# Performance work log

Hardware: AMD Instinct MI355X
Metric: run time of the kernel (lower is better)

## Reference

```python
import jax, jax.numpy as jnp
import numpy as np


def avg_pool_2x2(x):
    # x: [B, H, W, C] -> [B, H//2, W//2, C], non-overlapping 2x2 mean (Keras AveragePooling2D default)
    B, H, W, C = x.shape
    return x.reshape(B, H // 2, 2, W // 2, 2, C).mean(axis=(2, 4))


def setup_inputs() -> dict:
    key = jax.random.key(0)
    k1, k2, k3, k4, k5 = jax.random.split(key, 5)
    B, H, W, C = 16, 64, 64, 512
    x = jax.random.normal(k1, (B, H, W, C), dtype=jnp.float32)
    Wf = jax.random.normal(k2, (C, C // 8), dtype=jnp.float32) * 0.02
    Wg = jax.random.normal(k3, (C, C // 8), dtype=jnp.float32) * 0.02
    Wh = jax.random.normal(k4, (C, C // 2), dtype=jnp.float32) * 0.02
    Wo = jax.random.normal(k5, (C // 2, C), dtype=jnp.float32) * 0.02
    return {"x": x, "Wf": Wf, "Wg": Wg, "Wh": Wh, "Wo": Wo}


def reference(x, Wf, Wg, Wh, Wo):
    B, H, W, C = x.shape
    # 1x1 convs are per-pixel matmuls over channels
    f = jnp.einsum('bhwc,cd->bhwd', x, Wf).reshape(B, H * W, C // 8)          # queries
    xp = avg_pool_2x2(x)                                                      # [B,H/2,W/2,C]
    g = jnp.einsum('bhwc,cd->bhwd', xp, Wg).reshape(B, H * W // 4, C // 8)    # keys
    h = jnp.einsum('bhwc,cd->bhwd', xp, Wh).reshape(B, H * W // 4, C // 2)    # values
    attn = jax.nn.softmax(jnp.einsum('bqd,bkd->bqk', f, g), axis=-1)          # [B, HW, HW/4]
    y = jnp.einsum('bqk,bkd->bqd', attn, h).reshape(B, H, W, C // 2)
    out = jnp.einsum('bhwd,dc->bhwc', y, Wo) + x                              # residual
    return out
```

## Files before the change

kernel.cpp:

```cpp
#include <hip/hip_runtime.h>


#define DEVI static __device__ __forceinline__

typedef float f32x4  __attribute__((ext_vector_type(4)));
typedef float f32x16 __attribute__((ext_vector_type(16)));
typedef short bf16x8 __attribute__((ext_vector_type(8)));

DEVI short f2bf(float f) {
  union { float f; unsigned u; } v; v.f = f;
  unsigned r = v.u + 0x7FFFu + ((v.u >> 16) & 1u);
  return (short)(r >> 16);
}
DEVI float b2f(short s) {
  union { unsigned u; float f; } v; v.u = ((unsigned)(unsigned short)s) << 16; return v.f;
}
DEVI unsigned cvtpk(float lo, float hi) {
  unsigned r;
  asm("v_cvt_pk_bf16_f32 %0, %1, %2" : "=v"(r) : "v"(lo), "v"(hi));
  return r;
}
DEVI f32x4 mfma16(bf16x8 a, bf16x8 b, f32x4 c) {
  return __builtin_amdgcn_mfma_f32_16x16x32_bf16(a, b, c, 0, 0, 0);
}
DEVI f32x16 mfma32(bf16x8 a, bf16x8 b, f32x16 c) {
  return __builtin_amdgcn_mfma_f32_32x32x16_bf16(a, b, c, 0, 0, 0);
}
DEVI void gload16(const short* gsrc, short* lds) {
  __builtin_amdgcn_global_load_lds(
      (const __attribute__((address_space(1))) void*)gsrc,
      (__attribute__((address_space(3))) void*)lds, 16, 0, 0);
}

__global__ __launch_bounds__(256) void prep_weights(
    const float* __restrict__ Wf, const float* __restrict__ Wg,
    const float* __restrict__ Wh, const float* __restrict__ Wo,
    short* __restrict__ WfT, short* __restrict__ WgT,
    short* __restrict__ WhT, short* __restrict__ WoT) {
  int i = blockIdx.x * 256 + threadIdx.x;
  const float* src; short* dst; int K, N, e;
  if (i < 32768)       { src = Wf; dst = WfT; K = 512; N = 64;  e = i; }
  else if (i < 65536)  { src = Wg; dst = WgT; K = 512; N = 64;  e = i - 32768; }
  else if (i < 196608) { src = Wh; dst = WhT; K = 512; N = 256; e = i - 65536; }
  else                 { src = Wo; dst = WoT; K = 256; N = 512; e = i - 196608; }
  int n = e / K, k = e - n * K;
  dst[e] = f2bf(src[(long)k * N + n]);
}

template<bool SRC_F32>
DEVI void stage64(short* lds, const void* gsrc, int rows, int stride, int tid) {
  const int chunks = rows * 8;
  for (int c = tid; c < chunks; c += 256) {
    int row = c >> 3, slot = c & 7;
    int dstb = row*128 + ((slot ^ (row & 7)) << 4);
    if (SRC_F32) {
      const float* s = (const float*)gsrc + (long)row*stride + slot*8;
      float4 u0 = *(const float4*)s;
      float4 u1 = *(const float4*)(s + 4);
      union { unsigned u[4]; bf16x8 v; } pk;
      pk.u[0] = cvtpk(u0.x, u0.y); pk.u[1] = cvtpk(u0.z, u0.w);
      pk.u[2] = cvtpk(u1.x, u1.y); pk.u[3] = cvtpk(u1.z, u1.w);
      *(bf16x8*)((char*)lds + dstb) = pk.v;
    } else {
      *(bf16x8*)((char*)lds + dstb) =
          *(const bf16x8*)((const short*)gsrc + (long)row*stride + slot*8);
    }
  }
}

template<bool A_F32, bool POOL>
__global__ __launch_bounds__(256) void gemm_k512(const void* __restrict__ A,
    const short* __restrict__ BT, short* __restrict__ C, int Nfull,
    short* __restrict__ xp) {
  __shared__ short As[128*64];
  __shared__ short Bs[64*64];
  const int m0 = blockIdx.x * 128;
  const int n0 = blockIdx.y * 64;
  const int tid = threadIdx.x, w = tid >> 6, lane = tid & 63;
  const int l15 = lane & 15, lhi = lane >> 4;
  const int wr = w >> 1, wc = w & 1;
  f32x4 acc[4][2] = {};
  for (int kt = 0; kt < 8; ++kt) {
    const int k0 = kt * 64;
    if constexpr (A_F32)
      stage64<true >(As, (const float*)A + (long)m0*512 + k0, 128, 512, tid);
    else
      stage64<false>(As, (const short*)A + (long)m0*512 + k0, 128, 512, tid);
    stage64<false>(Bs, BT + (long)n0*512 + k0, 64, 512, tid);
    __syncthreads();
    if constexpr (POOL) {
      const long pr0 = (long)(m0 >> 12)*1024 + ((m0 & 4095) >> 7)*32;
      int wp = tid >> 3, cs = tid & 7;
      const char* Ab = (const char*)As;
      bf16x8 v00 = *(const bf16x8*)(Ab + (2*wp  )*128 + ((cs ^ ((2*wp  )&7))<<4));
      bf16x8 v01 = *(const bf16x8*)(Ab + (2*wp+1)*128 + ((cs ^ ((2*wp+1)&7))<<4));
      bf16x8 v10 = *(const bf16x8*)(Ab + (64+2*wp)*128 + ((cs ^ ((2*wp  )&7))<<4));
      bf16x8 v11 = *(const bf16x8*)(Ab + (65+2*wp)*128 + ((cs ^ ((2*wp+1)&7))<<4));
      float s[8];
      #pragma unroll
      for (int j = 0; j < 8; ++j)
        s[j] = 0.25f*(b2f(v00[j])+b2f(v01[j])+b2f(v10[j])+b2f(v11[j]));
      union { unsigned u[4]; bf16x8 v; } pk;
      pk.u[0] = cvtpk(s[0], s[1]); pk.u[1] = cvtpk(s[2], s[3]);
      pk.u[2] = cvtpk(s[4], s[5]); pk.u[3] = cvtpk(s[6], s[7]);
      *(bf16x8*)(xp + (pr0 + wp)*512 + k0 + cs*8) = pk.v;
    }
    bf16x8 af[4][2], bfr[2][2];
    #pragma unroll
    for (int mi = 0; mi < 4; ++mi)
      #pragma unroll
      for (int ks = 0; ks < 2; ++ks) {
        int m = wr*64 + mi*16 + l15;
        int slot = lhi + ks*4;
        af[mi][ks] = *(const bf16x8*)((const char*)As + m*128 + ((slot ^ (m & 7)) << 4));
      }
    #pragma unroll
    for (int ni = 0; ni < 2; ++ni)
      #pragma unroll
      for (int ks = 0; ks < 2; ++ks) {
        int n = wc*32 + ni*16 + l15;
        int slot = lhi + ks*4;
        bfr[ni][ks] = *(const bf16x8*)((const char*)Bs + n*128 + ((slot ^ (n & 7)) << 4));
      }
    #pragma unroll
    for (int ks = 0; ks < 2; ++ks)
      #pragma unroll
      for (int mi = 0; mi < 4; ++mi)
        #pragma unroll
        for (int ni = 0; ni < 2; ++ni)
          acc[mi][ni] = mfma16(af[mi][ks], bfr[ni][ks], acc[mi][ni]);
    __syncthreads();
  }
  #pragma unroll
  for (int mi = 0; mi < 4; ++mi)
    #pragma unroll
    for (int ni = 0; ni < 2; ++ni)
      #pragma unroll
      for (int r = 0; r < 4; ++r) {
        long row = m0 + wr*64 + mi*16 + lhi*4 + r;
        int col = n0 + wc*32 + ni*16 + l15;
        C[row * (long)Nfull + col] = f2bf(acc[mi][ni][r]);
      }
}

__global__ __launch_bounds__(256) void transpose_h(const short* __restrict__ h,
                                                   short* __restrict__ hT) {
  __shared__ short t[64][72];
  const int k0 = blockIdx.x * 64, n0 = blockIdx.y * 64, b = blockIdx.z;
  const int tid = threadIdx.x;
  {
    int row = tid >> 2, cch = (tid & 3) * 16;
    const short* src = h + ((long)b*1024 + k0 + row) * 256 + n0 + cch;
    *(bf16x8*)&t[row][cch]     = *(const bf16x8*)src;
    *(bf16x8*)&t[row][cch + 8] = *(const bf16x8*)(src + 8);
  }
  __syncthreads();
  {
    int n = tid >> 2, kch = (tid & 3) * 16;
    bf16x8 lo, hi;
    #pragma unroll
    for (int j = 0; j < 8; ++j) { lo[j] = t[kch + j][n]; hi[j] = t[kch + 8 + j][n]; }
    short* dst = hT + ((long)b*256 + n0 + n) * 1024 + k0 + kch;
    *(bf16x8*)dst       = lo;
    *(bf16x8*)(dst + 8) = hi;
  }
}

__global__ __launch_bounds__(256, 2) void attn_kernel(const short* __restrict__ f,
    const short* __restrict__ g, const short* __restrict__ hT,
    const short* __restrict__ WoT, const float* __restrict__ x,
    float* __restrict__ out) {
  extern __shared__ __align__(16) char smem[];
  const int b = blockIdx.y, q0 = blockIdx.x * 128;
  const int tid = threadIdx.x, w = tid >> 6, lane = tid & 63;
  const int l31 = lane & 31, hi = lane >> 5;

  bf16x8 fq[4];
  {
    const short* frow = f + ((long)b*4096 + q0 + w*32 + l31) * 64;
    #pragma unroll
    for (int ks = 0; ks < 4; ++ks) fq[ks] = *(const bf16x8*)(frow + ks*16 + hi*8);
  }

  f32x16 acc2[8] = {};
  float rsq = 0.f;

  auto stage = [&](int buf, int kt) {
    const int k0 = kt * 64;
    short* gbuf = (short*)(smem + buf*8192);
    short* hbuf = (short*)(smem + 16384 + buf*32768);
    #pragma unroll
    for (int it = 0; it < 2; ++it) {
      int c = it*256 + w*64 + lane;
      int row = c >> 3, gslot = (c & 7) ^ (row & 7);
      gload16(g + ((long)b*1024 + k0 + row)*64 + gslot*8, gbuf + (it*256 + w*64)*8);
    }
    #pragma unroll
    for (int it = 0; it < 8; ++it) {
      int c = it*256 + w*64 + lane;
      int row = c >> 3, gslot = (c & 7) ^ (row & 7);
      gload16(hT + ((long)b*256 + row)*1024 + k0 + gslot*8, hbuf + (it*256 + w*64)*8);
    }
  };

  stage(0, 0);
  int cur = 0;
  for (int kt = 0; kt < 16; ++kt) {
    if (kt < 15) {
      stage(cur ^ 1, kt + 1);
      asm volatile("s_waitcnt vmcnt(10)" ::: "memory");
    } else {
      asm volatile("s_waitcnt vmcnt(0)" ::: "memory");
    }
    __builtin_amdgcn_s_barrier();
    const char* gcur = (const char*)(smem + cur*8192);
    const char* hcur = (const char*)(smem + 16384 + cur*32768);
    bf16x8 pa[4];
    #pragma unroll
    for (int kc2 = 0; kc2 < 2; ++kc2) {
      f32x16 s2 = {};
      #pragma unroll
      for (int ks = 0; ks < 4; ++ks) {
        int key = kc2*32 + l31;
        bf16x8 gb = *(const bf16x8*)(gcur + key*128 + (((ks*2 + hi) ^ (l31 & 7)) << 4));
        s2 = mfma32(gb, fq[ks], s2);
      }
      #pragma unroll
      for (int fh = 0; fh < 2; ++fh) {
        const int G = fh*8;
        float e0 = __expf(s2[G+0]), e1 = __expf(s2[G+1]);
        float e2 = __expf(s2[G+2]), e3 = __expf(s2[G+3]);
        float e4 = __expf(s2[G+4]), e5 = __expf(s2[G+5]);
        float e6 = __expf(s2[G+6]), e7 = __expf(s2[G+7]);
        rsq += ((e0 + e1) + (e2 + e3)) + ((e4 + e5) + (e6 + e7));
        unsigned a0 = cvtpk(e0, e1), a1 = cvtpk(e2, e3);
        unsigned b0 = cvtpk(e4, e5), b1 = cvtpk(e6, e7);
        asm volatile("v_permlane32_swap_b32 %0, %1" : "+v"(b0), "+v"(a0));
        asm volatile("v_permlane32_swap_b32 %0, %1" : "+v"(b1), "+v"(a1));
        union { unsigned u[4]; bf16x8 v; } pk;
        pk.u[0] = a0; pk.u[1] = a1; pk.u[2] = b0; pk.u[3] = b1;
        pa[kc2*2 + fh] = pk.v;
      }
    }
    __builtin_amdgcn_s_setprio(1);
    #pragma unroll
    for (int ks = 0; ks < 4; ++ks) {
      #pragma unroll
      for (int nc2 = 0; nc2 < 8; ++nc2) {
        int n = nc2*32 + l31;
        bf16x8 hb = *(const bf16x8*)(hcur + n*128 + (((ks*2 + hi) ^ (l31 & 7)) << 4));
        acc2[nc2] = mfma32(hb, pa[ks], acc2[nc2]);
      }
    }
    __builtin_amdgcn_s_setprio(0);
    __builtin_amdgcn_s_barrier();
    cur ^= 1;
  }
  rsq += __shfl_xor(rsq, 32);
  float ri = 1.f / rsq;
  bf16x8 yB[16];
  #pragma unroll
  for (int nc2 = 0; nc2 < 8; ++nc2) {
    #pragma unroll
    for (int fh = 0; fh < 2; ++fh) {
      const int G = fh*8;
      unsigned a0 = cvtpk(acc2[nc2][G+0]*ri, acc2[nc2][G+1]*ri);
      unsigned a1 = cvtpk(acc2[nc2][G+2]*ri, acc2[nc2][G+3]*ri);
      unsigned b0 = cvtpk(acc2[nc2][G+4]*ri, acc2[nc2][G+5]*ri);
      unsigned b1 = cvtpk(acc2[nc2][G+6]*ri, acc2[nc2][G+7]*ri);
      asm volatile("v_permlane32_swap_b32 %0, %1" : "+v"(b0), "+v"(a0));
      asm volatile("v_permlane32_swap_b32 %0, %1" : "+v"(b1), "+v"(a1));
      union { unsigned u[4]; bf16x8 v; } pk;
      pk.u[0] = a0; pk.u[1] = a1; pk.u[2] = b0; pk.u[3] = b1;
      yB[nc2*2 + fh] = pk.v;
    }
  }
  const long qrow = (long)b*4096 + q0 + w*32 + l31;
  const float* xrow = x + qrow*512;
  float* orow = out + qrow*512;
  for (int cc2 = 0; cc2 < 16; ++cc2) {
    f32x16 ao0 = {}, ao1 = {};
    #pragma unroll
    for (int ns2 = 0; ns2 < 8; ++ns2) {
      bf16x8 wo0 = *(const bf16x8*)(WoT + (cc2*32 + l31)*256 + (2*ns2  )*16 + hi*8);
      bf16x8 wo1 = *(const bf16x8*)(WoT + (cc2*32 + l31)*256 + (2*ns2+1)*16 + hi*8);
      ao0 = mfma32(wo0, yB[2*ns2  ], ao0);
      ao1 = mfma32(wo1, yB[2*ns2+1], ao1);
    }
    #pragma unroll
    for (int g2 = 0; g2 < 4; ++g2) {
      int c = cc2*32 + g2*8 + hi*4;
      float4 xv = *(const float4*)(xrow + c);
      float4 ov;
      ov.x = ao0[g2*4+0] + ao1[g2*4+0] + xv.x;
      ov.y = ao0[g2*4+1] + ao1[g2*4+1] + xv.y;
      ov.z = ao0[g2*4+2] + ao1[g2*4+2] + xv.z;
      ov.w = ao0[g2*4+3] + ao1[g2*4+3] + xv.w;
      *(float4*)(orow + c) = ov;
    }
  }
}

extern "C" void kernel_launch(void* const* d_in, const int* in_sizes, int n_in,
                              void* d_out, int out_size, void* d_ws, size_t ws_size,
                              hipStream_t stream) {
  const float* x  = (const float*)d_in[0];
  const float* Wf = (const float*)d_in[1];
  const float* Wg = (const float*)d_in[2];
  const float* Wh = (const float*)d_in[3];
  const float* Wo = (const float*)d_in[4];
  float* out = (float*)d_out;

  short* xp  = (short*)d_ws;
  short* fb  = xp  + (long)16*1024*512;
  short* gb  = fb  + (long)65536*64;
  short* hb  = gb  + (long)16384*64;
  short* hTb = hb  + (long)16384*256;
  short* WfT = hTb + (long)16*256*1024;
  short* WgT = WfT + 64*512;
  short* WhT = WgT + 64*512;
  short* WoT = WhT + 256*512;

  hipFuncSetAttribute((const void*)attn_kernel,
                      hipFuncAttributeMaxDynamicSharedMemorySize, 81920);

  prep_weights<<<1536, 256, 0, stream>>>(Wf, Wg, Wh, Wo, WfT, WgT, WhT, WoT);
  gemm_k512<true , true ><<<dim3(512, 1), 256, 0, stream>>>((const void*)x,  WfT, fb, 64,  xp);
  gemm_k512<false, false><<<dim3(128, 1), 256, 0, stream>>>((const void*)xp, WgT, gb, 64,  nullptr);
  gemm_k512<false, false><<<dim3(128, 4), 256, 0, stream>>>((const void*)xp, WhT, hb, 256, nullptr);
  transpose_h <<<dim3(16, 4, 16), 256, 0, stream>>>(hb, hTb);
  attn_kernel <<<dim3(32, 16), 256, 81920, stream>>>(fb, gb, hTb, WoT, x, out);
}
```

Measured before the change: 203.2 us.

## Split output projection into separate GEMM kernel and fold log2e into queries

The Wo projection and residual add move out of the attention kernel into a new gemm_out kernel. The attention kernel now writes the normalized y as bf16 to a workspace buffer, and gemm_out stages y tiles in LDS, preloads Wo fragments and prefetches the x residual. The query projection output is also scaled by log2(e), so the softmax can use exp2f instead of __expf. This is meant to shorten the attention kernel's tail and improve overlap in the projection, at the cost of an extra y round trip through memory and one more kernel launch.

New measurement: 258.4 us. 1.27x slower.

```diff
diff --git a/kernel.cpp b/kernel.cpp
--- a/kernel.cpp
+++ b/kernel.cpp
@@ -71,7 +71,7 @@
 template<bool A_F32, bool POOL>
 __global__ __launch_bounds__(256) void gemm_k512(const void* __restrict__ A,
     const short* __restrict__ BT, short* __restrict__ C, int Nfull,
-    short* __restrict__ xp) {
+    short* __restrict__ xp, float cscale) {
   __shared__ short As[128*64];
   __shared__ short Bs[64*64];
   const int m0 = blockIdx.x * 128;
@@ -139,7 +139,7 @@
       for (int r = 0; r < 4; ++r) {
         long row = m0 + wr*64 + mi*16 + lhi*4 + r;
         int col = n0 + wc*32 + ni*16 + l15;
-        C[row * (long)Nfull + col] = f2bf(acc[mi][ni][r]);
+        C[row * (long)Nfull + col] = f2bf(acc[mi][ni][r] * cscale);
       }
 }
 
@@ -168,8 +168,7 @@
 
 __global__ __launch_bounds__(256, 2) void attn_kernel(const short* __restrict__ f,
     const short* __restrict__ g, const short* __restrict__ hT,
-    const short* __restrict__ WoT, const float* __restrict__ x,
-    float* __restrict__ out) {
+    short* __restrict__ y) {
   extern __shared__ __align__(16) char smem[];
   const int b = blockIdx.y, q0 = blockIdx.x * 128;
   const int tid = threadIdx.x, w = tid >> 6, lane = tid & 63;
@@ -228,10 +227,10 @@
       #pragma unroll
       for (int fh = 0; fh < 2; ++fh) {
         const int G = fh*8;
-        float e0 = __expf(s2[G+0]), e1 = __expf(s2[G+1]);
-        float e2 = __expf(s2[G+2]), e3 = __expf(s2[G+3]);
-        float e4 = __expf(s2[G+4]), e5 = __expf(s2[G+5]);
-        float e6 = __expf(s2[G+6]), e7 = __expf(s2[G+7]);
+        float e0 = exp2f(s2[G+0]), e1 = exp2f(s2[G+1]);
+        float e2 = exp2f(s2[G+2]), e3 = exp2f(s2[G+3]);
+        float e4 = exp2f(s2[G+4]), e5 = exp2f(s2[G+5]);
+        float e6 = exp2f(s2[G+6]), e7 = exp2f(s2[G+7]);
         rsq += ((e0 + e1) + (e2 + e3)) + ((e4 + e5) + (e6 + e7));
         unsigned a0 = cvtpk(e0, e1), a1 = cvtpk(e2, e3);
         unsigned b0 = cvtpk(e4, e5), b1 = cvtpk(e6, e7);
@@ -258,7 +257,8 @@
   }
   rsq += __shfl_xor(rsq, 32);
   float ri = 1.f / rsq;
-  bf16x8 yB[16];
+  const long qrow = (long)b*4096 + q0 + w*32 + l31;
+  short* yrow = y + qrow*256;
   #pragma unroll
   for (int nc2 = 0; nc2 < 8; ++nc2) {
     #pragma unroll
@@ -272,31 +272,66 @@
       asm volatile("v_permlane32_swap_b32 %0, %1" : "+v"(b1), "+v"(a1));
       union { unsigned u[4]; bf16x8 v; } pk;
       pk.u[0] = a0; pk.u[1] = a1; pk.u[2] = b0; pk.u[3] = b1;
-      yB[nc2*2 + fh] = pk.v;
-    }
-  }
-  const long qrow = (long)b*4096 + q0 + w*32 + l31;
+      *(bf16x8*)(yrow + (nc2*2 + fh)*16 + hi*8) = pk.v;
+    }
+  }
+}
+
+__global__ __launch_bounds__(256) void gemm_out(const short* __restrict__ y,
+    const short* __restrict__ WoT, const float* __restrict__ x,
+    float* __restrict__ out) {
+  __shared__ short ys[128*256];
+  const int q0 = blockIdx.x * 128;
+  const int tid = threadIdx.x, w = tid >> 6, lane = tid & 63;
+  const int l31 = lane & 31, hi = lane >> 5;
+  #pragma unroll
+  for (int it = 0; it < 16; ++it) {
+    int c = it*256 + w*64 + lane;
+    int row = c >> 5, gslot = (c & 31) ^ (row & 31);
+    gload16(y + ((long)q0 + row)*256 + gslot*8, (short*)ys + (it*256 + w*64)*8);
+  }
+  asm volatile("s_waitcnt vmcnt(0)" ::: "memory");
+  __builtin_amdgcn_s_barrier();
+  const int qr = w*32 + l31;
+  bf16x8 yB[16];
+  #pragma unroll
+  for (int ks = 0; ks < 16; ++ks) {
+    int slot = (ks*2 + hi) ^ (qr & 31);
+    yB[ks] = *(const bf16x8*)((const char*)ys + qr*512 + slot*16);
+  }
+  const long qrow = (long)q0 + qr;
   const float* xrow = x + qrow*512;
   float* orow = out + qrow*512;
+  float4 xcur[4], xnxt[4];
+  #pragma unroll
+  for (int g2 = 0; g2 < 4; ++g2) xcur[g2] = *(const float4*)(xrow + g2*8 + hi*4);
+  #pragma unroll
+  for (int g2 = 0; g2 < 4; ++g2) xnxt[g2] = *(const float4*)(xrow + 32 + g2*8 + hi*4);
   for (int cc2 = 0; cc2 < 16; ++cc2) {
+    bf16x8 wo[16];
+    const short* wrow = WoT + ((long)cc2*32 + l31)*256 + hi*8;
+    #pragma unroll
+    for (int ns = 0; ns < 16; ++ns) wo[ns] = *(const bf16x8*)(wrow + ns*16);
     f32x16 ao0 = {}, ao1 = {};
     #pragma unroll
     for (int ns2 = 0; ns2 < 8; ++ns2) {
-      bf16x8 wo0 = *(const bf16x8*)(WoT + (cc2*32 + l31)*256 + (2*ns2  )*16 + hi*8);
-      bf16x8 wo1 = *(const bf16x8*)(WoT + (cc2*32 + l31)*256 + (2*ns2+1)*16 + hi*8);
-      ao0 = mfma32(wo0, yB[2*ns2  ], ao0);
-      ao1 = mfma32(wo1, yB[2*ns2+1], ao1);
+      ao0 = mfma32(wo[2*ns2  ], yB[2*ns2  ], ao0);
+      ao1 = mfma32(wo[2*ns2+1], yB[2*ns2+1], ao1);
     }
     #pragma unroll
     for (int g2 = 0; g2 < 4; ++g2) {
       int c = cc2*32 + g2*8 + hi*4;
-      float4 xv = *(const float4*)(xrow + c);
       float4 ov;
-      ov.x = ao0[g2*4+0] + ao1[g2*4+0] + xv.x;
-      ov.y = ao0[g2*4+1] + ao1[g2*4+1] + xv.y;
-      ov.z = ao0[g2*4+2] + ao1[g2*4+2] + xv.z;
-      ov.w = ao0[g2*4+3] + ao1[g2*4+3] + xv.w;
+      ov.x = ao0[g2*4+0] + ao1[g2*4+0] + xcur[g2].x;
+      ov.y = ao0[g2*4+1] + ao1[g2*4+1] + xcur[g2].y;
+      ov.z = ao0[g2*4+2] + ao1[g2*4+2] + xcur[g2].z;
+      ov.w = ao0[g2*4+3] + ao1[g2*4+3] + xcur[g2].w;
       *(float4*)(orow + c) = ov;
+    }
+    #pragma unroll
+    for (int g2 = 0; g2 < 4; ++g2) {
+      xcur[g2] = xnxt[g2];
+      if (cc2 < 14) xnxt[g2] = *(const float4*)(xrow + (cc2+2)*32 + g2*8 + hi*4);
     }
   }
 }
@@ -316,7 +351,8 @@
   short* gb  = fb  + (long)65536*64;
   short* hb  = gb  + (long)16384*64;
   short* hTb = hb  + (long)16384*256;
-  short* WfT = hTb + (long)16*256*1024;
+  short* yb  = hTb + (long)16*256*1024;
+  short* WfT = yb  + (long)65536*256;
   short* WgT = WfT + 64*512;
   short* WhT = WgT + 64*512;
   short* WoT = WhT + 256*512;
@@ -324,10 +360,12 @@
   hipFuncSetAttribute((const void*)attn_kernel,
                       hipFuncAttributeMaxDynamicSharedMemorySize, 81920);
 
+  const float LOG2E = 1.44269504f;
   prep_weights<<<1536, 256, 0, stream>>>(Wf, Wg, Wh, Wo, WfT, WgT, WhT, WoT);
-  gemm_k512<true , true ><<<dim3(512, 1), 256, 0, stream>>>((const void*)x,  WfT, fb, 64,  xp);
-  gemm_k512<false, false><<<dim3(128, 1), 256, 0, stream>>>((const void*)xp, WgT, gb, 64,  nullptr);
-  gemm_k512<false, false><<<dim3(128, 4), 256, 0, stream>>>((const void*)xp, WhT, hb, 256, nullptr);
+  gemm_k512<true , true ><<<dim3(512, 1), 256, 0, stream>>>((const void*)x,  WfT, fb, 64,  xp, LOG2E);
+  gemm_k512<false, false><<<dim3(128, 1), 256, 0, stream>>>((const void*)xp, WgT, gb, 64,  nullptr, 1.0f);
+  gemm_k512<false, false><<<dim3(128, 4), 256, 0, stream>>>((const void*)xp, WhT, hb, 256, nullptr, 1.0f);
   transpose_h <<<dim3(16, 4, 16), 256, 0, stream>>>(hb, hTb);
-  attn_kernel <<<dim3(32, 16), 256, 81920, stream>>>(fb, gb, hTb, WoT, x, out);
-}
+  attn_kernel <<<dim3(32, 16), 256, 81920, stream>>>(fb, gb, hTb, yb);
+  gemm_out    <<<512, 256, 0, stream>>>(yb, WoT, x, out);
+}
```
